# Kernel optimization log

Measured on AMD Instinct MI355X. Metric: run time of the kernel, lower is better.

## Reference

```python
import jax, jax.numpy as jnp
import numpy as np

B, N, D = 8, 2048, 512

def setup_inputs() -> dict:
    key = jax.random.key(0)
    k1, k2, k3, k4, k5 = jax.random.split(key, 5)
    s = 1.0 / np.sqrt(D)
    return {
        "x": jax.random.normal(k1, (B, N, D), dtype=jnp.float32),
        "w_qkv": jax.random.normal(k2, (D, 3 * D), dtype=jnp.float32) * s,
        "b_qkv": jax.random.normal(k3, (3 * D,), dtype=jnp.float32) * 0.01,
        "w_fc": jax.random.normal(k4, (D, D), dtype=jnp.float32) * s,
        "b_fc": jax.random.normal(k5, (D,), dtype=jnp.float32) * 0.01,
    }

def reference(x, w_qkv, b_qkv, w_fc, b_fc):
    scale = 1.0 / (x.shape[-1] ** 0.5)
    qkv = x @ w_qkv + b_qkv                      # [B, N, 3D]
    q, k, v = jnp.split(qkv, 3, axis=-1)         # each [B, N, D]
    attn = jnp.einsum("bnd,bmd->bnm", q, k) * scale
    attn = jax.nn.softmax(attn, axis=-1)
    out = jnp.einsum("bnm,bmd->bnd", attn, v)
    return out @ w_fc + b_fc + x
```

## Files before the change

### kernel.cpp

```cpp
#include <hip/hip_runtime.h>
#include <stdint.h>

typedef unsigned short u16;
typedef unsigned int u32;
typedef __attribute__((ext_vector_type(8))) short short8;
typedef __attribute__((ext_vector_type(4))) float f32x4;
typedef __attribute__((ext_vector_type(8))) unsigned short u16x8;
typedef __attribute__((ext_vector_type(4))) float float4_t;

__device__ __forceinline__ float b2f(u16 u) { return __uint_as_float(((u32)u) << 16); }
__device__ __forceinline__ u16 f2b(float f) {
  u32 u = __float_as_uint(f);
  u += 0x7fffu + ((u >> 16) & 1u);
  return (u16)(u >> 16);
}

typedef const __attribute__((address_space(1))) void* gas_t;
typedef __attribute__((address_space(3))) void* las_t;
__device__ __forceinline__ void gl_lds16(const void* g, void* l) {
  __builtin_amdgcn_global_load_lds((gas_t)(uintptr_t)g, (las_t)(u32)(uintptr_t)l, 16, 0, 0);
}
__device__ __forceinline__ void barrier_pin() {
  __builtin_amdgcn_sched_barrier(0);
  __builtin_amdgcn_s_barrier();
  __builtin_amdgcn_sched_barrier(0);
}
__device__ __forceinline__ void lgkm0_pin() {
  asm volatile("s_waitcnt lgkmcnt(0)" ::: "memory");
  __builtin_amdgcn_sched_barrier(0);
}

__global__ __launch_bounds__(256) void cvt_f2b_kernel(const float* __restrict__ src,
                                                      u16* __restrict__ dst, long n) {
  long i = ((long)blockIdx.x * 256 + threadIdx.x) * 8;
  if (i >= n) return;
  float4_t v0 = *(const float4_t*)(src + i);
  float4_t v1 = *(const float4_t*)(src + i + 4);
  u16x8 o;
#pragma unroll
  for (int j = 0; j < 4; ++j) { o[j] = f2b(v0[j]); o[4 + j] = f2b(v1[j]); }
  *(u16x8*)(dst + i) = o;
}

__global__ __launch_bounds__(256) void tr_cvt2(const float* __restrict__ w1,
                                               u16* __restrict__ d1,
                                               const float* __restrict__ w2,
                                               u16* __restrict__ d2) {
  const int zz = blockIdx.z;
  if (zz == 1 && blockIdx.x >= 16) return;
  const float* src = zz ? w2 : w1;
  u16* dst = zz ? d2 : d1;
  const int C = zz ? 512 : 1536;
  const int R = 512;
  __shared__ float t[32][33];
  const int bx = blockIdx.x * 32;
  const int by = blockIdx.y * 32;
  const int tx = threadIdx.x & 31, ty = threadIdx.x >> 5;
#pragma unroll
  for (int i = 0; i < 32; i += 8)
    t[ty + i][tx] = src[(long)(by + ty + i) * C + bx + tx];
  __syncthreads();
#pragma unroll
  for (int i = 0; i < 32; i += 8)
    dst[(long)(bx + ty + i) * R + by + tx] = f2b(t[tx][ty + i]);
}

__global__ __launch_bounds__(256) void tr_v(const u16* __restrict__ qkv, u16* __restrict__ vt) {
  __shared__ u16 t[32][33];
  const int b = blockIdx.z;
  const int r0 = blockIdx.x * 32;
  const int d0 = blockIdx.y * 32;
  const int tx = threadIdx.x & 31, ty = threadIdx.x >> 5;
#pragma unroll
  for (int i = 0; i < 32; i += 8)
    t[ty + i][tx] = qkv[((long)b * 2048 + r0 + ty + i) * 1536 + 1024 + d0 + tx];
  __syncthreads();
#pragma unroll
  for (int i = 0; i < 32; i += 8)
    vt[((long)b * 512 + d0 + ty + i) * 2048 + r0 + tx] = t[tx][ty + i];
}

template <bool OUT_F32, bool BIAS, bool RES, bool EXP_EPI, bool ROWSUM_DIV>
__global__ __launch_bounds__(512, 4)
void gemm128(const u16* __restrict__ A, const u16* __restrict__ Bt, void* __restrict__ Cv,
             const float* __restrict__ bias, const float* __restrict__ res,
             int K, int lda, int ldb, int ldc,
             long aStride, long bStride, long cStride, float alpha) {
  __shared__ u16 As[2][128 * 64];
  __shared__ u16 Bs[2][128 * 64];
  __shared__ float lsum[ROWSUM_DIV ? 128 : 1];
  const int tid = threadIdx.x;
  const int wid = tid >> 6, lane = tid & 63;
  const int wr = wid >> 2, wc = wid & 3;
  const int lr = lane & 15, lg = lane >> 4;

  const int gx = gridDim.x, gy = gridDim.y;
  int id = (blockIdx.z * gy + blockIdx.y) * gx + blockIdx.x;
  const int nwg = gx * gy * gridDim.z;
  id = (id & 7) * (nwg >> 3) + (id >> 3);
  const int bxi = id % gx;
  const int t2 = id / gx;
  const int byi = t2 % gy;
  const long z = t2 / gy;

  A += z * aStride;
  Bt += z * bStride;
  const int by = byi * 128;
  const int bx = bxi * 128;

  f32x4 acc[4][2] = {};
  f32x4 acc_l[4] = {};
  short8 ah[4][2], bh[2][2];
  short8 ones;
#pragma unroll
  for (int j = 0; j < 8; ++j) ones[j] = (short)0x3F80;

  const int w8l = wid * 8 + (lane >> 3);
  const int scol_src = ((lane & 7) ^ (lane >> 3)) * 8;
  const int scol_lin = (lane & 7) * 8;
  const int nT = K >> 6;
  const int sx = lane & 7;

  auto stage = [&](int kt) {
    const int bb = kt & 1;
    const long kc = (long)kt * 64 + scol_src;
#pragma unroll
    for (int r = 0; r < 2; ++r) {
      const int row = r * 64 + w8l;
      gl_lds16(A + (long)(by + row) * lda + kc, &As[bb][row * 64 + scol_lin]);
    }
#pragma unroll
    for (int r = 0; r < 2; ++r) {
      const int row = r * 64 + w8l;
      gl_lds16(Bt + (long)(bx + row) * ldb + kc, &Bs[bb][row * 64 + scol_lin]);
    }
  };

  stage(0);
  asm volatile("s_waitcnt vmcnt(0)" ::: "memory");
  barrier_pin();

  for (int T = 0; T < nT; ++T) {
    const int bb = T & 1;
    const bool more = (T + 1) < nT;
    if (more) stage(T + 1);
#pragma unroll
    for (int mi = 0; mi < 4; ++mi)
#pragma unroll
      for (int ks = 0; ks < 2; ++ks)
        ah[mi][ks] = *(const short8*)&As[bb][(wr * 64 + mi * 16 + lr) * 64 +
                                             (((ks * 4 + lg) ^ sx) * 8)];
#pragma unroll
    for (int n = 0; n < 2; ++n)
#pragma unroll
      for (int ks = 0; ks < 2; ++ks)
        bh[n][ks] = *(const short8*)&Bs[bb][(wc * 32 + n * 16 + lr) * 64 +
                                            (((ks * 4 + lg) ^ sx) * 8)];
    lgkm0_pin();
    __builtin_amdgcn_s_setprio(1);
#pragma unroll
    for (int mi = 0; mi < 4; ++mi)
#pragma unroll
      for (int n = 0; n < 2; ++n)
#pragma unroll
        for (int ks = 0; ks < 2; ++ks)
          acc[mi][n] = __builtin_amdgcn_mfma_f32_16x16x32_bf16(
              ah[mi][ks], bh[n][ks], acc[mi][n], 0, 0, 0);
    if constexpr (ROWSUM_DIV) {
      if (wc == 0) {
#pragma unroll
        for (int mi = 0; mi < 4; ++mi)
#pragma unroll
          for (int ks = 0; ks < 2; ++ks)
            acc_l[mi] = __builtin_amdgcn_mfma_f32_16x16x32_bf16(
                ah[mi][ks], ones, acc_l[mi], 0, 0, 0);
      }
    }
    __builtin_amdgcn_s_setprio(0);
    if (more) asm volatile("s_waitcnt vmcnt(0)" ::: "memory");
    barrier_pin();
  }

  if constexpr (ROWSUM_DIV) {
    if (wc == 0 && lr == 0) {
#pragma unroll
      for (int mi = 0; mi < 4; ++mi)
#pragma unroll
        for (int j = 0; j < 4; ++j)
          lsum[wr * 64 + mi * 16 + lg * 4 + j] = acc_l[mi][j];
    }
    __syncthreads();
  }

  if constexpr (EXP_EPI) {
    u16* C = (u16*)Cv + z * cStride;
#pragma unroll
    for (int mi = 0; mi < 4; ++mi)
#pragma unroll
      for (int ni = 0; ni < 2; ++ni)
#pragma unroll
        for (int j = 0; j < 4; ++j) {
          const long row = by + wr * 64 + mi * 16 + lg * 4 + j;
          const int col = bx + wc * 32 + ni * 16 + lr;
          C[row * (long)ldc + col] = f2b(exp2f(acc[mi][ni][j] * alpha));
        }
  } else if constexpr (OUT_F32) {
    float* C = (float*)Cv + z * cStride;
#pragma unroll
    for (int mi = 0; mi < 4; ++mi)
#pragma unroll
      for (int ni = 0; ni < 2; ++ni)
#pragma unroll
        for (int j = 0; j < 4; ++j) {
          const long row = by + wr * 64 + mi * 16 + lg * 4 + j;
          const int col = bx + wc * 32 + ni * 16 + lr;
          float v = acc[mi][ni][j] * alpha;
          if (BIAS) v += bias[col];
          if (RES) v += res[row * (long)ldc + col];
          C[row * (long)ldc + col] = v;
        }
  } else {
    u16* C = (u16*)Cv + z * cStride;
#pragma unroll
    for (int mi = 0; mi < 4; ++mi)
#pragma unroll
      for (int j = 0; j < 4; ++j) {
        float invl = 1.0f;
        if constexpr (ROWSUM_DIV) invl = 1.0f / lsum[wr * 64 + mi * 16 + lg * 4 + j];
#pragma unroll
        for (int ni = 0; ni < 2; ++ni) {
          const long row = by + wr * 64 + mi * 16 + lg * 4 + j;
          const int col = bx + wc * 32 + ni * 16 + lr;
          float v = acc[mi][ni][j] * alpha;
          if constexpr (ROWSUM_DIV) v *= invl;
          if (BIAS) v += bias[col];
          C[row * (long)ldc + col] = f2b(v);
        }
      }
  }
}

extern "C" void kernel_launch(void* const* d_in, const int* in_sizes, int n_in,
                              void* d_out, int out_size, void* d_ws, size_t ws_size,
                              hipStream_t stream) {
  const float* x = (const float*)d_in[0];
  const float* w_qkv = (const float*)d_in[1];
  const float* b_qkv = (const float*)d_in[2];
  const float* w_fc = (const float*)d_in[3];
  const float* b_fc = (const float*)d_in[4];
  float* out = (float*)d_out;

  char* ws = (char*)d_ws;
  const long MT = 16384;
  u16* xb = (u16*)(ws);
  u16* wqkvT = (u16*)(ws + 16777216);
  u16* wfcT = (u16*)(ws + 18350080);
  u16* qkv = (u16*)(ws + 18874368);
  u16* vt = (u16*)(ws + 69206016);
  u16* S = (u16*)(ws + 85983232);
  u16* attn = xb;

  const float alpha2 = 0.04419417382415922f * 1.4426950408889634f;

  cvt_f2b_kernel<<<4096, 256, 0, stream>>>(x, xb, MT * 512);
  tr_cvt2<<<dim3(48, 16, 2), 256, 0, stream>>>(w_qkv, wqkvT, w_fc, wfcT);

  gemm128<false, true, false, false, false><<<dim3(12, 128, 1), 512, 0, stream>>>(
      xb, wqkvT, qkv, b_qkv, nullptr,
      512, 512, 512, 1536, 0, 0, 0, 1.0f);

  tr_v<<<dim3(64, 16, 8), 256, 0, stream>>>(qkv, vt);

  gemm128<false, false, false, true, false><<<dim3(16, 16, 8), 512, 0, stream>>>(
      qkv, qkv + 512, S, nullptr, nullptr,
      512, 1536, 1536, 2048,
      (long)2048 * 1536, (long)2048 * 1536, (long)2048 * 2048, alpha2);

  gemm128<false, false, false, false, true><<<dim3(4, 16, 8), 512, 0, stream>>>(
      S, vt, attn, nullptr, nullptr,
      2048, 2048, 2048, 512,
      (long)2048 * 2048, (long)512 * 2048, (long)2048 * 512, 1.0f);

  gemm128<true, true, true, false, false><<<dim3(4, 128, 1), 512, 0, stream>>>(
      attn, wfcT, out, b_fc, x,
      512, 512, 512, 512, 0, 0, 0, 1.0f);
}
```

Measured before the change: 163.5 us.

## Defer softmax row normalization to output projection and vectorize V transpose

```diff
diff --git a/kernel.cpp b/kernel.cpp
--- a/kernel.cpp
+++ b/kernel.cpp
@@ -65,30 +65,32 @@
     dst[(long)(bx + ty + i) * R + by + tx] = f2b(t[tx][ty + i]);
 }
 
-__global__ __launch_bounds__(256) void tr_v(const u16* __restrict__ qkv, u16* __restrict__ vt) {
-  __shared__ u16 t[32][33];
+__global__ __launch_bounds__(512) void tr_v(const u16* __restrict__ qkv,
+                                            u16* __restrict__ vt) {
+  __shared__ u16 t[64][66];
   const int b = blockIdx.z;
-  const int r0 = blockIdx.x * 32;
-  const int d0 = blockIdx.y * 32;
-  const int tx = threadIdx.x & 31, ty = threadIdx.x >> 5;
-#pragma unroll
-  for (int i = 0; i < 32; i += 8)
-    t[ty + i][tx] = qkv[((long)b * 2048 + r0 + ty + i) * 1536 + 1024 + d0 + tx];
+  const int r0 = blockIdx.x * 64;
+  const int d0 = blockIdx.y * 64;
+  const int tr = threadIdx.x >> 3;
+  const int tc = (threadIdx.x & 7) * 8;
+  *(u16x8*)&t[tr][tc] =
+      *(const u16x8*)&qkv[((long)b * 2048 + r0 + tr) * 1536 + 1024 + d0 + tc];
   __syncthreads();
-#pragma unroll
-  for (int i = 0; i < 32; i += 8)
-    vt[((long)b * 512 + d0 + ty + i) * 2048 + r0 + tx] = t[tx][ty + i];
-}
-
-template <bool OUT_F32, bool BIAS, bool RES, bool EXP_EPI, bool ROWSUM_DIV>
+  u16x8 o;
+#pragma unroll
+  for (int j = 0; j < 8; ++j) o[j] = t[tc + j][tr];
+  *(u16x8*)&vt[((long)b * 512 + d0 + tr) * 2048 + r0 + tc] = o;
+}
+
+template <bool OUT_F32, bool BIAS, bool RES, bool EXP_EPI, bool ROWSUM_ST, bool DIVROW>
 __global__ __launch_bounds__(512, 4)
 void gemm128(const u16* __restrict__ A, const u16* __restrict__ Bt, void* __restrict__ Cv,
              const float* __restrict__ bias, const float* __restrict__ res,
+             float* __restrict__ lglob, const float* __restrict__ lin,
              int K, int lda, int ldb, int ldc,
              long aStride, long bStride, long cStride, float alpha) {
   __shared__ u16 As[2][128 * 64];
   __shared__ u16 Bs[2][128 * 64];
-  __shared__ float lsum[ROWSUM_DIV ? 128 : 1];
   const int tid = threadIdx.x;
   const int wid = tid >> 6, lane = tid & 63;
   const int wr = wid >> 2, wc = wid & 3;
@@ -108,6 +110,8 @@
   const int by = byi * 128;
   const int bx = bxi * 128;
 
+  const bool do_l = ROWSUM_ST && (bxi == 0);
+
   f32x4 acc[4][2] = {};
   f32x4 acc_l[4] = {};
   short8 ah[4][2], bh[2][2];
@@ -166,8 +170,8 @@
         for (int ks = 0; ks < 2; ++ks)
           acc[mi][n] = __builtin_amdgcn_mfma_f32_16x16x32_bf16(
               ah[mi][ks], bh[n][ks], acc[mi][n], 0, 0, 0);
-    if constexpr (ROWSUM_DIV) {
-      if (wc == 0) {
+    if constexpr (ROWSUM_ST) {
+      if (do_l && wc == 0) {
 #pragma unroll
         for (int mi = 0; mi < 4; ++mi)
 #pragma unroll
@@ -181,15 +185,14 @@
     barrier_pin();
   }
 
-  if constexpr (ROWSUM_DIV) {
-    if (wc == 0 && lr == 0) {
+  if constexpr (ROWSUM_ST) {
+    if (do_l && wc == 0 && lr == 0) {
 #pragma unroll
       for (int mi = 0; mi < 4; ++mi)
 #pragma unroll
         for (int j = 0; j < 4; ++j)
-          lsum[wr * 64 + mi * 16 + lg * 4 + j] = acc_l[mi][j];
-    }
-    __syncthreads();
+          lglob[z * 2048 + by + wr * 64 + mi * 16 + lg * 4 + j] = acc_l[mi][j];
+    }
   }
 
   if constexpr (EXP_EPI) {
@@ -209,6 +212,25 @@
 #pragma unroll
     for (int mi = 0; mi < 4; ++mi)
 #pragma unroll
+      for (int j = 0; j < 4; ++j) {
+        const long row = by + wr * 64 + mi * 16 + lg * 4 + j;
+        float invl = 1.0f;
+        if constexpr (DIVROW) invl = 1.0f / lin[row];
+#pragma unroll
+        for (int ni = 0; ni < 2; ++ni) {
+          const int col = bx + wc * 32 + ni * 16 + lr;
+          float v = acc[mi][ni][j] * alpha;
+          if constexpr (DIVROW) v = acc[mi][ni][j] * invl;
+          if (BIAS) v += bias[col];
+          if (RES) v += res[row * (long)ldc + col];
+          C[row * (long)ldc + col] = v;
+        }
+      }
+  } else {
+    u16* C = (u16*)Cv + z * cStride;
+#pragma unroll
+    for (int mi = 0; mi < 4; ++mi)
+#pragma unroll
       for (int ni = 0; ni < 2; ++ni)
 #pragma unroll
         for (int j = 0; j < 4; ++j) {
@@ -216,27 +238,8 @@
           const int col = bx + wc * 32 + ni * 16 + lr;
           float v = acc[mi][ni][j] * alpha;
           if (BIAS) v += bias[col];
-          if (RES) v += res[row * (long)ldc + col];
-          C[row * (long)ldc + col] = v;
-        }
-  } else {
-    u16* C = (u16*)Cv + z * cStride;
-#pragma unroll
-    for (int mi = 0; mi < 4; ++mi)
-#pragma unroll
-      for (int j = 0; j < 4; ++j) {
-        float invl = 1.0f;
-        if constexpr (ROWSUM_DIV) invl = 1.0f / lsum[wr * 64 + mi * 16 + lg * 4 + j];
-#pragma unroll
-        for (int ni = 0; ni < 2; ++ni) {
-          const long row = by + wr * 64 + mi * 16 + lg * 4 + j;
-          const int col = bx + wc * 32 + ni * 16 + lr;
-          float v = acc[mi][ni][j] * alpha;
-          if constexpr (ROWSUM_DIV) v *= invl;
-          if (BIAS) v += bias[col];
           C[row * (long)ldc + col] = f2b(v);
         }
-      }
   }
 }
 
@@ -259,29 +262,30 @@
   u16* vt = (u16*)(ws + 69206016);
   u16* S = (u16*)(ws + 85983232);
   u16* attn = xb;
+  float* lvec = (float*)(ws + 16777216);
 
   const float alpha2 = 0.04419417382415922f * 1.4426950408889634f;
 
   cvt_f2b_kernel<<<4096, 256, 0, stream>>>(x, xb, MT * 512);
   tr_cvt2<<<dim3(48, 16, 2), 256, 0, stream>>>(w_qkv, wqkvT, w_fc, wfcT);
 
-  gemm128<false, true, false, false, false><<<dim3(12, 128, 1), 512, 0, stream>>>(
-      xb, wqkvT, qkv, b_qkv, nullptr,
+  gemm128<false, true, false, false, false, false><<<dim3(12, 128, 1), 512, 0, stream>>>(
+      xb, wqkvT, qkv, b_qkv, nullptr, nullptr, nullptr,
       512, 512, 512, 1536, 0, 0, 0, 1.0f);
 
-  tr_v<<<dim3(64, 16, 8), 256, 0, stream>>>(qkv, vt);
-
-  gemm128<false, false, false, true, false><<<dim3(16, 16, 8), 512, 0, stream>>>(
-      qkv, qkv + 512, S, nullptr, nullptr,
+  tr_v<<<dim3(32, 8, 8), 512, 0, stream>>>(qkv, vt);
+
+  gemm128<false, false, false, true, false, false><<<dim3(16, 16, 8), 512, 0, stream>>>(
+      qkv, qkv + 512, S, nullptr, nullptr, nullptr, nullptr,
       512, 1536, 1536, 2048,
       (long)2048 * 1536, (long)2048 * 1536, (long)2048 * 2048, alpha2);
 
-  gemm128<false, false, false, false, true><<<dim3(4, 16, 8), 512, 0, stream>>>(
-      S, vt, attn, nullptr, nullptr,
+  gemm128<false, false, false, false, true, false><<<dim3(4, 16, 8), 512, 0, stream>>>(
+      S, vt, attn, nullptr, nullptr, lvec, nullptr,
       2048, 2048, 2048, 512,
       (long)2048 * 2048, (long)512 * 2048, (long)2048 * 512, 1.0f);
 
-  gemm128<true, true, true, false, false><<<dim3(4, 128, 1), 512, 0, stream>>>(
-      attn, wfcT, out, b_fc, x,
+  gemm128<true, true, true, false, false, true><<<dim3(4, 128, 1), 512, 0, stream>>>(
+      attn, wfcT, out, b_fc, x, nullptr, lvec,
       512, 512, 512, 512, 0, 0, 0, 1.0f);
 }
```

Result: no change. 160.3 us (-1.9%).
